# Kernel optimization log

Hardware: AMD Instinct MI355X
Metric: run time of the kernel (lower is better)

Reference implementation:

```python
import jax, jax.numpy as jnp
import numpy as np

NUM_EMBEDDINGS = 8192
EMBEDDING_DIM = 256
COMMITMENT_COST = 0.25


def setup_inputs() -> dict:
    key = jax.random.key(0)
    k1, k2 = jax.random.split(key)
    inputs = jax.random.normal(k1, (16, 2048, EMBEDDING_DIM), dtype=jnp.float32)
    # codebook initialized uniform(-1/K, 1/K) as in the torch module
    codebook = jax.random.uniform(
        k2, (NUM_EMBEDDINGS, EMBEDDING_DIM), dtype=jnp.float32,
        minval=-1.0 / NUM_EMBEDDINGS, maxval=1.0 / NUM_EMBEDDINGS)
    return {"inputs": inputs, "codebook": codebook}


def reference(inputs, codebook):
    B, T, D = inputs.shape
    flat = inputs.reshape(-1, D)                      # [BT, D]
    distances = (
        jnp.sum(flat * flat, axis=1, keepdims=True)
        + jnp.sum(codebook * codebook, axis=1)
        - 2.0 * jnp.matmul(flat, codebook.T)
    )
    idx = jnp.argmin(distances, axis=1)               # [BT]
    quantized = codebook[idx].reshape(B, T, D)        # gather == one-hot @ codebook
    e_latent_loss = jnp.mean((jax.lax.stop_gradient(quantized) - inputs) ** 2)
    q_latent_loss = jnp.mean((quantized - jax.lax.stop_gradient(inputs)) ** 2)
    loss = q_latent_loss + COMMITMENT_COST * e_latent_loss
    # straight-through estimator
    quantized_st = inputs + jax.lax.stop_gradient(quantized - inputs)
    return quantized_st, idx.reshape(B, T), loss
```

## Files before the change

kernel.cpp:

```cpp
#include <hip/hip_runtime.h>
#include <hip/hip_bf16.h>
#include <stdint.h>

#define D      256
#define K      8192
#define NROWS  32768
#define QELEMS 8388608

typedef __attribute__((ext_vector_type(8))) short bf16x8;
typedef __attribute__((ext_vector_type(4))) float f32x4;
typedef unsigned int u32;
typedef unsigned short u16;

__device__ __forceinline__ u16 f2bf(float f) {
    u32 b = __float_as_uint(f);
    return (u16)((b + 0x7fffu + ((b >> 16) & 1u)) >> 16);
}

__global__ __launch_bounds__(256) void vq_prep_kernel(
    const float* __restrict__ cb, u16* __restrict__ ch,
    float* __restrict__ se, float* __restrict__ loss_sum) {
    int row = blockIdx.x * 4 + (threadIdx.x >> 6);
    int l = threadIdx.x & 63;
    float4 v = *(const float4*)(cb + (size_t)row * D + l * 4);
    ushort4 o;
    o.x = f2bf(v.x); o.y = f2bf(v.y); o.z = f2bf(v.z); o.w = f2bf(v.w);
    *(ushort4*)(ch + (size_t)row * D + l * 4) = o;
    float s = v.x * v.x + v.y * v.y + v.z * v.z + v.w * v.w;
    #pragma unroll
    for (int off = 32; off > 0; off >>= 1) s += __shfl_down(s, off, 64);
    if (l == 0) se[row] = s;
    if (blockIdx.x == 0 && threadIdx.x == 0) *loss_sum = 0.f;
}

__global__ __launch_bounds__(512) void vq_filter_kernel(
    const u16* __restrict__ ch, const float* __restrict__ x,
    const float* __restrict__ se, u32* __restrict__ cand)
{
    __shared__ u16 xf[32768];
    __shared__ u16 As[32768];

    const int tid  = threadIdx.x;
    const int lane = tid & 63;
    const int wave = tid >> 6;
    const int m_w  = wave >> 1;
    const int n_w  = wave & 1;
    const int l15  = lane & 15;
    const int l4   = lane >> 4;
    const int row0 = blockIdx.x * 128;

    #pragma unroll
    for (int i = 0; i < 8; ++i) {
        int e  = tid + i * 512;
        int q  = e >> 6, le = e & 63;
        int rl = (q >> 3) * 16 + (le & 15);
        int kk = (q & 7) * 32 + (le >> 4) * 8;
        const float* xp = x + (size_t)(row0 + rl) * D + kk;
        float4 a = *(const float4*)xp;
        float4 b = *(const float4*)(xp + 4);
        bf16x8 f;
        f[0] = (short)f2bf(a.x); f[1] = (short)f2bf(a.y);
        f[2] = (short)f2bf(a.z); f[3] = (short)f2bf(a.w);
        f[4] = (short)f2bf(b.x); f[5] = (short)f2bf(b.y);
        f[6] = (short)f2bf(b.z); f[7] = (short)f2bf(b.w);
        *(bf16x8*)(xf + (size_t)e * 8) = f;
    }

    float b0[4], b1[4]; int c0[4], c1[4];
    #pragma unroll
    for (int nt = 0; nt < 4; ++nt) { b0[nt] = 1e30f; b1[nt] = 1e30f; c0[nt] = 0; c1[nt] = 0; }

    const u16* xfb = xf + (size_t)(n_w * 4 * 8 * 64 + lane) * 8;

    #pragma unroll 1
    for (int ct = 0; ct < 64; ++ct) {
        const int k0 = ct << 7;

        __syncthreads();
        #pragma unroll
        for (int i = 0; i < 8; ++i) {
            int g  = wave * 8 + i;
            int c  = g >> 3;
            int mg = g & 7;
            const u16* gp = ch + (size_t)(k0 + mg * 16 + l15) * D + c * 32 + l4 * 8;
            u16* lb = As + (size_t)((c * 8 + mg) * 64) * 8;
            __builtin_amdgcn_global_load_lds(
                (const __attribute__((address_space(1))) u32*)gp,
                (__attribute__((address_space(3))) u32*)lb, 16, 0, 0);
        }
        __syncthreads();

        f32x4 acc[2][4];
        #pragma unroll
        for (int mt = 0; mt < 2; ++mt)
            #pragma unroll
            for (int nt = 0; nt < 4; ++nt) acc[mt][nt] = (f32x4){0.f, 0.f, 0.f, 0.f};

        #pragma unroll
        for (int c = 0; c < 8; ++c) {
            bf16x8 Af0 = *(const bf16x8*)(As + (size_t)((c * 8 + m_w * 2 + 0) * 64 + lane) * 8);
            bf16x8 Af1 = *(const bf16x8*)(As + (size_t)((c * 8 + m_w * 2 + 1) * 64 + lane) * 8);
            #pragma unroll
            for (int nt = 0; nt < 4; ++nt) {
                bf16x8 Bv = *(const bf16x8*)(xfb + (size_t)((nt * 8 + c) * 64) * 8);
                acc[0][nt] = __builtin_amdgcn_mfma_f32_16x16x32_bf16(Af0, Bv, acc[0][nt], 0, 0, 0);
                acc[1][nt] = __builtin_amdgcn_mfma_f32_16x16x32_bf16(Af1, Bv, acc[1][nt], 0, 0, 0);
            }
        }

        f32x4 sev[2];
        #pragma unroll
        for (int mt = 0; mt < 2; ++mt)
            sev[mt] = *(const f32x4*)(se + k0 + (m_w * 2 + mt) * 16 + l4 * 4);

        #pragma unroll
        for (int nt = 0; nt < 4; ++nt) {
            float tmn = 1e30f;
            #pragma unroll
            for (int mt = 0; mt < 2; ++mt)
                #pragma unroll
                for (int r = 0; r < 4; ++r)
                    tmn = fminf(tmn, fmaf(-2.f, acc[mt][nt][r], sev[mt][r]));
            if (tmn < b1[nt]) {
                #pragma unroll
                for (int mt = 0; mt < 2; ++mt)
                    #pragma unroll
                    for (int r = 0; r < 4; ++r) {
                        float t = fmaf(-2.f, acc[mt][nt][r], sev[mt][r]);
                        int  cv = k0 + (m_w * 2 + mt) * 16 + l4 * 4 + r;
                        bool in0 = t < b0[nt];
                        bool in1 = t < b1[nt];
                        float ob0 = b0[nt]; int oc0 = c0[nt];
                        b1[nt] = in0 ? ob0 : (in1 ? t  : b1[nt]);
                        c1[nt] = in0 ? oc0 : (in1 ? cv : c1[nt]);
                        b0[nt] = in0 ? t  : ob0;
                        c0[nt] = in0 ? cv : oc0;
                    }
            }
        }
    }

    #pragma unroll
    for (int nt = 0; nt < 4; ++nt) {
        int row = row0 + n_w * 64 + nt * 16 + l15;
        int sl  = (m_w * 4 + l4) * 2;
        cand[(size_t)row * 32 + sl]     = (u32)c0[nt];
        cand[(size_t)row * 32 + sl + 1] = (u32)c1[nt];
    }
}

__global__ __launch_bounds__(1024) void vq_rescore_kernel(
    const float* __restrict__ x, const float* __restrict__ cb,
    const float* __restrict__ se, const u32* __restrict__ cand,
    float* __restrict__ out, float* __restrict__ loss_sum)
{
    const int wave = threadIdx.x >> 6;
    const int lane = threadIdx.x & 63;
    const int row  = blockIdx.x * 16 + wave;

    float4 xv = *(const float4*)(x + (size_t)row * D + lane * 4);
    float sx = xv.x * xv.x + xv.y * xv.y + xv.z * xv.z + xv.w * xv.w;
    #pragma unroll
    for (int o = 1; o < 64; o <<= 1) sx += __shfl_xor(sx, o, 64);

    u32 myc = cand[(size_t)row * 32 + (lane & 31)];
    float best = 1e30f; int bk = 0x7fffffff;
    #pragma unroll 4
    for (int j = 0; j < 32; ++j) {
        int code = __shfl((int)myc, j, 64);
        float4 ev = *(const float4*)(cb + (size_t)code * D + lane * 4);
        float p = xv.x * ev.x + xv.y * ev.y + xv.z * ev.z + xv.w * ev.w;
        #pragma unroll
        for (int o = 1; o < 64; o <<= 1) p += __shfl_xor(p, o, 64);
        float dist = (sx + se[code]) - 2.0f * p;
        if (dist < best || (dist == best && code < bk)) { best = dist; bk = code; }
    }

    float4 q = *(const float4*)(cb + (size_t)bk * D + lane * 4);
    *(float4*)(out + (size_t)row * D + lane * 4) = q;
    float dx = q.x - xv.x, dy = q.y - xv.y, dz = q.z - xv.z, dw = q.w - xv.w;
    float s = dx * dx + dy * dy + dz * dz + dw * dw;
    #pragma unroll
    for (int o = 1; o < 64; o <<= 1) s += __shfl_xor(s, o, 64);
    if (lane == 0) out[QELEMS + row] = (float)bk;

    __shared__ float red[16];
    if (lane == 0) red[wave] = s;
    __syncthreads();
    if (threadIdx.x == 0) {
        float t = 0.f;
        #pragma unroll
        for (int w2 = 0; w2 < 16; ++w2) t += red[w2];
        atomicAdd(loss_sum, t);
    }
}

__global__ void vq_fin_kernel(const float* __restrict__ loss_sum, float* __restrict__ out) {
    out[QELEMS + NROWS] = 1.25f * (*loss_sum) * (1.0f / (float)QELEMS);
}

extern "C" void kernel_launch(void* const* d_in, const int* in_sizes, int n_in,
                              void* d_out, int out_size, void* d_ws, size_t ws_size,
                              hipStream_t stream) {
    const float* x  = (const float*)d_in[0];
    const float* cb = (const float*)d_in[1];
    float* out = (float*)d_out;

    u16* ch = (u16*)d_out;

    char* ws = (char*)d_ws;
    float* loss_sum = (float*)ws;
    float* sebuf    = (float*)(ws + 4096);
    u32*   cand     = (u32*)(ws + 65536);

    vq_prep_kernel<<<K / 4, 256, 0, stream>>>(cb, ch, sebuf, loss_sum);
    vq_filter_kernel<<<NROWS / 128, 512, 0, stream>>>(ch, x, sebuf, cand);
    vq_rescore_kernel<<<NROWS / 16, 1024, 0, stream>>>(x, cb, sebuf, cand, out, loss_sum);
    vq_fin_kernel<<<1, 1, 0, stream>>>(loss_sum, out);
}
```

Baseline: 456.1 us.

## Double-buffer codebook tiles, keep input fragments in registers, halve rescore candidates

The filter kernel now uses 64-row blocks of 256 threads. Each block holds its bf16 input fragments in registers instead of LDS, and streams 64-code codebook tiles into a double-buffered LDS region so the next tile's load overlaps the current MFMA work. With fewer M-waves per block, each row keeps 16 top-2 candidates instead of 32, which halves the fp32 rescore loop. Fewer candidates raises the risk of missing the true argmin under bf16 error, and more register pressure may limit occupancy.

New measurement: 393.5 us. -13.7%, faster.

```diff
diff --git a/kernel.cpp b/kernel.cpp
--- a/kernel.cpp
+++ b/kernel.cpp
@@ -33,79 +33,86 @@
     if (blockIdx.x == 0 && threadIdx.x == 0) *loss_sum = 0.f;
 }
 
-__global__ __launch_bounds__(512) void vq_filter_kernel(
+__global__ __launch_bounds__(256) void vq_filter_kernel(
     const u16* __restrict__ ch, const float* __restrict__ x,
     const float* __restrict__ se, u32* __restrict__ cand)
 {
-    __shared__ u16 xf[32768];
-    __shared__ u16 As[32768];
+    __shared__ u16 As[2][16384];
 
     const int tid  = threadIdx.x;
     const int lane = tid & 63;
     const int wave = tid >> 6;
-    const int m_w  = wave >> 1;
-    const int n_w  = wave & 1;
+    const int m_w  = wave & 1;
+    const int n_w  = wave >> 1;
     const int l15  = lane & 15;
     const int l4   = lane >> 4;
-    const int row0 = blockIdx.x * 128;
+    const int row0 = blockIdx.x * 64;
+
+    bf16x8 Bf[2][8];
+    #pragma unroll
+    for (int nt = 0; nt < 2; ++nt) {
+        const float* xr = x + (size_t)(row0 + n_w * 32 + nt * 16 + l15) * D + l4 * 8;
+        #pragma unroll
+        for (int c = 0; c < 8; ++c) {
+            float4 a = *(const float4*)(xr + c * 32);
+            float4 b = *(const float4*)(xr + c * 32 + 4);
+            bf16x8 f;
+            f[0] = (short)f2bf(a.x); f[1] = (short)f2bf(a.y);
+            f[2] = (short)f2bf(a.z); f[3] = (short)f2bf(a.w);
+            f[4] = (short)f2bf(b.x); f[5] = (short)f2bf(b.y);
+            f[6] = (short)f2bf(b.z); f[7] = (short)f2bf(b.w);
+            Bf[nt][c] = f;
+        }
+    }
+
+    float b0[2], b1[2]; int c0[2], c1[2];
+    #pragma unroll
+    for (int nt = 0; nt < 2; ++nt) { b0[nt] = 1e30f; b1[nt] = 1e30f; c0[nt] = 0; c1[nt] = 0; }
 
     #pragma unroll
     for (int i = 0; i < 8; ++i) {
-        int e  = tid + i * 512;
-        int q  = e >> 6, le = e & 63;
-        int rl = (q >> 3) * 16 + (le & 15);
-        int kk = (q & 7) * 32 + (le >> 4) * 8;
-        const float* xp = x + (size_t)(row0 + rl) * D + kk;
-        float4 a = *(const float4*)xp;
-        float4 b = *(const float4*)(xp + 4);
-        bf16x8 f;
-        f[0] = (short)f2bf(a.x); f[1] = (short)f2bf(a.y);
-        f[2] = (short)f2bf(a.z); f[3] = (short)f2bf(a.w);
-        f[4] = (short)f2bf(b.x); f[5] = (short)f2bf(b.y);
-        f[6] = (short)f2bf(b.z); f[7] = (short)f2bf(b.w);
-        *(bf16x8*)(xf + (size_t)e * 8) = f;
-    }
-
-    float b0[4], b1[4]; int c0[4], c1[4];
-    #pragma unroll
-    for (int nt = 0; nt < 4; ++nt) { b0[nt] = 1e30f; b1[nt] = 1e30f; c0[nt] = 0; c1[nt] = 0; }
-
-    const u16* xfb = xf + (size_t)(n_w * 4 * 8 * 64 + lane) * 8;
-
+        int g = wave * 8 + i;
+        const u16* gp = ch + (size_t)((g & 3) * 16 + l15) * D + (g >> 2) * 32 + l4 * 8;
+        u16* lb = &As[0][(size_t)g * 512];
+        __builtin_amdgcn_global_load_lds(
+            (const __attribute__((address_space(1))) u32*)gp,
+            (__attribute__((address_space(3))) u32*)lb, 16, 0, 0);
+    }
+    __syncthreads();
+
+    int buf = 0;
     #pragma unroll 1
-    for (int ct = 0; ct < 64; ++ct) {
-        const int k0 = ct << 7;
-
-        __syncthreads();
-        #pragma unroll
-        for (int i = 0; i < 8; ++i) {
-            int g  = wave * 8 + i;
-            int c  = g >> 3;
-            int mg = g & 7;
-            const u16* gp = ch + (size_t)(k0 + mg * 16 + l15) * D + c * 32 + l4 * 8;
-            u16* lb = As + (size_t)((c * 8 + mg) * 64) * 8;
-            __builtin_amdgcn_global_load_lds(
-                (const __attribute__((address_space(1))) u32*)gp,
-                (__attribute__((address_space(3))) u32*)lb, 16, 0, 0);
-        }
-        __syncthreads();
-
-        f32x4 acc[2][4];
+    for (int ct = 0; ct < 128; ++ct) {
+        const int k0 = ct << 6;
+
+        if (ct + 1 < 128) {
+            const int kn = (ct + 1) << 6;
+            #pragma unroll
+            for (int i = 0; i < 8; ++i) {
+                int g = wave * 8 + i;
+                const u16* gp = ch + (size_t)(kn + (g & 3) * 16 + l15) * D + (g >> 2) * 32 + l4 * 8;
+                u16* lb = &As[buf ^ 1][(size_t)g * 512];
+                __builtin_amdgcn_global_load_lds(
+                    (const __attribute__((address_space(1))) u32*)gp,
+                    (__attribute__((address_space(3))) u32*)lb, 16, 0, 0);
+            }
+        }
+
+        const u16* cb_t = &As[buf][0];
+        f32x4 acc[2][2];
         #pragma unroll
         for (int mt = 0; mt < 2; ++mt)
             #pragma unroll
-            for (int nt = 0; nt < 4; ++nt) acc[mt][nt] = (f32x4){0.f, 0.f, 0.f, 0.f};
+            for (int nt = 0; nt < 2; ++nt) acc[mt][nt] = (f32x4){0.f, 0.f, 0.f, 0.f};
 
         #pragma unroll
         for (int c = 0; c < 8; ++c) {
-            bf16x8 Af0 = *(const bf16x8*)(As + (size_t)((c * 8 + m_w * 2 + 0) * 64 + lane) * 8);
-            bf16x8 Af1 = *(const bf16x8*)(As + (size_t)((c * 8 + m_w * 2 + 1) * 64 + lane) * 8);
-            #pragma unroll
-            for (int nt = 0; nt < 4; ++nt) {
-                bf16x8 Bv = *(const bf16x8*)(xfb + (size_t)((nt * 8 + c) * 64) * 8);
-                acc[0][nt] = __builtin_amdgcn_mfma_f32_16x16x32_bf16(Af0, Bv, acc[0][nt], 0, 0, 0);
-                acc[1][nt] = __builtin_amdgcn_mfma_f32_16x16x32_bf16(Af1, Bv, acc[1][nt], 0, 0, 0);
-            }
+            bf16x8 Af0 = *(const bf16x8*)(cb_t + (size_t)((c * 4 + m_w * 2 + 0) * 64 + lane) * 8);
+            bf16x8 Af1 = *(const bf16x8*)(cb_t + (size_t)((c * 4 + m_w * 2 + 1) * 64 + lane) * 8);
+            acc[0][0] = __builtin_amdgcn_mfma_f32_16x16x32_bf16(Af0, Bf[0][c], acc[0][0], 0, 0, 0);
+            acc[0][1] = __builtin_amdgcn_mfma_f32_16x16x32_bf16(Af0, Bf[1][c], acc[0][1], 0, 0, 0);
+            acc[1][0] = __builtin_amdgcn_mfma_f32_16x16x32_bf16(Af1, Bf[0][c], acc[1][0], 0, 0, 0);
+            acc[1][1] = __builtin_amdgcn_mfma_f32_16x16x32_bf16(Af1, Bf[1][c], acc[1][1], 0, 0, 0);
         }
 
         f32x4 sev[2];
@@ -114,7 +121,7 @@
             sev[mt] = *(const f32x4*)(se + k0 + (m_w * 2 + mt) * 16 + l4 * 4);
 
         #pragma unroll
-        for (int nt = 0; nt < 4; ++nt) {
+        for (int nt = 0; nt < 2; ++nt) {
             float tmn = 1e30f;
             #pragma unroll
             for (int mt = 0; mt < 2; ++mt)
@@ -138,14 +145,17 @@
                     }
             }
         }
-    }
-
-    #pragma unroll
-    for (int nt = 0; nt < 4; ++nt) {
-        int row = row0 + n_w * 64 + nt * 16 + l15;
+
+        __syncthreads();
+        buf ^= 1;
+    }
+
+    #pragma unroll
+    for (int nt = 0; nt < 2; ++nt) {
+        int row = row0 + n_w * 32 + nt * 16 + l15;
         int sl  = (m_w * 4 + l4) * 2;
-        cand[(size_t)row * 32 + sl]     = (u32)c0[nt];
-        cand[(size_t)row * 32 + sl + 1] = (u32)c1[nt];
+        cand[(size_t)row * 16 + sl]     = (u32)c0[nt];
+        cand[(size_t)row * 16 + sl + 1] = (u32)c1[nt];
     }
 }
 
@@ -163,10 +173,10 @@
     #pragma unroll
     for (int o = 1; o < 64; o <<= 1) sx += __shfl_xor(sx, o, 64);
 
-    u32 myc = cand[(size_t)row * 32 + (lane & 31)];
+    u32 myc = cand[(size_t)row * 16 + (lane & 15)];
     float best = 1e30f; int bk = 0x7fffffff;
     #pragma unroll 4
-    for (int j = 0; j < 32; ++j) {
+    for (int j = 0; j < 16; ++j) {
         int code = __shfl((int)myc, j, 64);
         float4 ev = *(const float4*)(cb + (size_t)code * D + lane * 4);
         float p = xv.x * ev.x + xv.y * ev.y + xv.z * ev.z + xv.w * ev.w;
@@ -214,7 +224,7 @@
     u32*   cand     = (u32*)(ws + 65536);
 
     vq_prep_kernel<<<K / 4, 256, 0, stream>>>(cb, ch, sebuf, loss_sum);
-    vq_filter_kernel<<<NROWS / 128, 512, 0, stream>>>(ch, x, sebuf, cand);
+    vq_filter_kernel<<<NROWS / 64, 256, 0, stream>>>(ch, x, sebuf, cand);
     vq_rescore_kernel<<<NROWS / 16, 1024, 0, stream>>>(x, cb, sebuf, cand, out, loss_sum);
     vq_fin_kernel<<<1, 1, 0, stream>>>(loss_sum, out);
 }
```
